# Optimization experiments

Measured on AMD Instinct MI355X. Metric: run time of the kernel, lower is better.

The kernel has to match this reference:

```python
import jax, jax.numpy as jnp
import numpy as np

HIDDEN_DIM = 64
EIGS_DIM = 16
N_LAYERS = 2
NUM_USERS = 100000
NUM_ITEMS = 200000
N_NODES = NUM_USERS + NUM_ITEMS
N_EDGES = 1250000
N_PATHS = 14  # 2**(sample_hop+1) - 2 with sample_hop=3
LN_EPS = 1e-5


def setup_inputs() -> dict:
    key = jax.random.key(0)
    k1, k2, k3, k4, k5 = jax.random.split(key, 5)
    return {
        "user_emb": 0.1 * jax.random.normal(k1, (NUM_USERS, HIDDEN_DIM), dtype=jnp.float32),
        "item_emb": 0.1 * jax.random.normal(k2, (NUM_ITEMS, HIDDEN_DIM), dtype=jnp.float32),
        "eigs": jax.random.normal(k3, (N_NODES, EIGS_DIM), dtype=jnp.float32),
        "lambda0": jnp.zeros((N_LAYERS,), dtype=jnp.float32),
        "path_emb_w": jnp.zeros((N_LAYERS, N_PATHS, 1), dtype=jnp.float32),
        "indices": jax.random.randint(k4, (2, N_EDGES), 0, N_NODES, dtype=jnp.int64)
        if jax.config.jax_enable_x64
        else jax.random.randint(k4, (2, N_EDGES), 0, N_NODES, dtype=jnp.int32),
        "path_type": jax.random.randint(k5, (N_EDGES,), 0, N_PATHS, dtype=jnp.int32),
    }


def _layer_norm(x, eps=LN_EPS):
    mu = jnp.mean(x, axis=-1, keepdims=True)
    var = jnp.var(x, axis=-1, keepdims=True)
    return (x - mu) * jax.lax.rsqrt(var + eps)


def _sparse_softmax(row, s, num_nodes):
    # softmax over edges grouped by target-node row index
    m = jax.ops.segment_max(s, row, num_segments=num_nodes)
    e = jnp.exp(s - m[row])
    denom = jax.ops.segment_sum(e, row, num_segments=num_nodes)
    return e / denom[row]


def _attention(y, eigs, row, col, path_type, lam0, pemb):
    sqrt_dim = 1.0 / jnp.sqrt(jnp.float32(HIDDEN_DIM))
    # per-edge q.k score  [E]
    x = jnp.sum(y[row] * y[col], axis=-1) * sqrt_dim
    yeig = jnp.sum(eigs[row] * eigs[col], axis=-1)
    s0 = x + jnp.exp(lam0) * yeig
    s1 = pemb[path_type, 0]
    a0 = _sparse_softmax(row, s0, N_NODES)
    a1 = _sparse_softmax(row, s1, N_NODES)
    a = 0.5 * (a0 + a1)
    # sparse-dense matmul: out[r] = sum_e a_e * v[col_e]
    return jax.ops.segment_sum(a[:, None] * y[col], row, num_segments=N_NODES)


def reference(user_emb, item_emb, eigs, lambda0, path_emb_w, indices, path_type):
    row, col = indices[0], indices[1]
    all_emb = jnp.concatenate([user_emb, item_emb], axis=0)  # [N, d]
    embs = [all_emb]
    for l in range(N_LAYERS):
        y = _layer_norm(all_emb)
        all_emb = _attention(y, eigs, row, col, path_type, lambda0[l], path_emb_w[l])
        embs.append(all_emb)
    light_out = jnp.mean(jnp.stack(embs, axis=1), axis=1)  # [N, d]
    return light_out
```

## Files before the change

### kernel.cpp

```cpp
#include <hip/hip_runtime.h>
#include <hip/hip_bf16.h>

#define HD 64
#define ED 16
#define NU 100000
#define NI 200000
#define NN 300000
#define NE 1250000
#define NP 14

#define RB 512
#define NBKT ((NN + RB - 1) / RB)
#define NR8 (NBKT * RB)
#define BCAP 2432
#define A_ITEMS 8
#define A_CHUNK (256 * A_ITEMS)
#define A_BLOCKS ((NE + A_CHUNK - 1) / A_CHUNK)
#define DBINS 64
#define IT 4

typedef __hip_bfloat16 bf16;
typedef unsigned short ushort8v __attribute__((ext_vector_type(8)));
typedef float  float4v __attribute__((ext_vector_type(4)));
typedef float  float2v __attribute__((ext_vector_type(2)));
typedef int    int2v   __attribute__((ext_vector_type(2)));

__device__ __forceinline__ float bf2f(unsigned short u) {
    union { unsigned int i; float f; } c; c.i = ((unsigned int)u) << 16; return c.f;
}
__device__ __forceinline__ unsigned short f2b(float x) {
    bf16 h = __float2bfloat16(x);
    unsigned short u; __builtin_memcpy(&u, &h, 2); return u;
}

__global__ void ln_kernel(const float* __restrict__ user_emb,
                          const float* __restrict__ item_emb,
                          bf16* __restrict__ yb)
{
    const int tid = blockIdx.x * blockDim.x + threadIdx.x;
    const int r   = tid >> 3;
    const int sub = tid & 7;
    if (r >= NN) return;
    const float* src = (r < NU) ? user_emb + (size_t)r * HD
                                : item_emb + (size_t)(r - NU) * HD;
    const float4 lo = *reinterpret_cast<const float4*>(src + sub * 8);
    const float4 hi = *reinterpret_cast<const float4*>(src + sub * 8 + 4);
    float x[8] = {lo.x, lo.y, lo.z, lo.w, hi.x, hi.y, hi.z, hi.w};

    float sm = 0.0f, sq = 0.0f;
#pragma unroll
    for (int j = 0; j < 8; ++j) { sm += x[j]; sq += x[j] * x[j]; }
    sm += __shfl_xor(sm, 1, 64); sq += __shfl_xor(sq, 1, 64);
    sm += __shfl_xor(sm, 2, 64); sq += __shfl_xor(sq, 2, 64);
    sm += __shfl_xor(sm, 4, 64); sq += __shfl_xor(sq, 4, 64);
    const float mu  = sm * (1.0f / 64.0f);
    const float var = sq * (1.0f / 64.0f) - mu * mu;
    const float inv = rsqrtf(var + 1e-5f);

    ushort8v w;
#pragma unroll
    for (int j = 0; j < 8; ++j) w[j] = f2b((x[j] - mu) * inv);
    *reinterpret_cast<ushort8v*>(yb + (size_t)r * HD + sub * 8) = w;
}

__global__ void bkt_scatter_kernel(const int* __restrict__ row,
                                   const int* __restrict__ col,
                                   const int* __restrict__ pt,
                                   int* __restrict__ wq_bkt,
                                   int* __restrict__ pairs)
{
    __shared__ int hist[NBKT];
    __shared__ int rbase[NBKT];
    __shared__ int roff[NBKT];
    const int tid = threadIdx.x;
    for (int j = tid; j < NBKT; j += 256) { hist[j] = 0; roff[j] = 0; }
    __syncthreads();

    const int base = blockIdx.x * A_CHUNK;
#pragma unroll
    for (int i = 0; i < A_ITEMS; ++i) {
        const int idx = base + i * 256 + tid;
        if (idx < NE) atomicAdd(&hist[row[idx] >> 9], 1);
    }
    __syncthreads();
    for (int j = tid; j < NBKT; j += 256) {
        const int h = hist[j];
        if (h) rbase[j] = atomicAdd(&wq_bkt[j], h);
    }
    __syncthreads();
#pragma unroll
    for (int i = 0; i < A_ITEMS; ++i) {
        const int idx = base + i * 256 + tid;
        if (idx < NE) {
            const int r = row[idx];
            const int b = r >> 9;
            const int v = col[idx] | (pt[idx] << 19) | ((r & (RB - 1)) << 23);
            const int o   = atomicAdd(&roff[b], 1);
            const int rel = rbase[b] + o;
            if (rel < BCAP) pairs[(size_t)b * BCAP + rel] = v;
        }
    }
}

__global__ __launch_bounds__(512)
void bkt_sort_kernel(const int* __restrict__ wq_bkt,
                     const int* __restrict__ pairs,
                     const float* __restrict__ eigs,
                     int2* __restrict__ rinfo,
                     int2* __restrict__ epacked)
{
    __shared__ int rcnt[RB], lrp[RB], wq2[RB], ssum[RB];
    __shared__ int dhist[DBINS], dbase[DBINS];
    __shared__ int perml[RB];
    __shared__ float estage[RB * ED];
    const int tid  = threadIdx.x;
    const int b    = blockIdx.x;
    const int r0   = b * RB;
    const int sbase = b * BCAP;
    int cntb = wq_bkt[b]; if (cntb > BCAP) cntb = BCAP;

    rcnt[tid] = 0; wq2[tid] = 0; perml[tid] = -1;
    if (tid < DBINS) dhist[tid] = 0;
    for (int k = tid; k < RB * ED; k += 512) {
        const int g = r0 * ED + k;
        estage[k] = (g < NN * ED) ? eigs[g] : 0.0f;
    }
    __syncthreads();

    for (int i = tid; i < cntb; i += 512)
        atomicAdd(&rcnt[(pairs[sbase + i] >> 23) & (RB - 1)], 1);
    __syncthreads();

    const int myc = rcnt[tid];
    ssum[tid] = myc;
    __syncthreads();
    for (int off = 1; off < RB; off <<= 1) {
        int x = (tid >= off) ? ssum[tid - off] : 0;
        __syncthreads();
        ssum[tid] += x;
        __syncthreads();
    }
    lrp[tid] = ssum[tid] - myc;
    __syncthreads();

    const int ra  = r0 + tid;
    const int bin = (DBINS - 1) - ((myc < DBINS - 1) ? myc : (DBINS - 1));
    if (ra < NN) atomicAdd(&dhist[bin], 1);
    __syncthreads();
    if (tid < DBINS) ssum[tid] = dhist[tid];
    __syncthreads();
    for (int off = 1; off < DBINS; off <<= 1) {
        int x = (tid < DBINS && tid >= off) ? ssum[tid - off] : 0;
        __syncthreads();
        if (tid < DBINS) ssum[tid] += x;
        __syncthreads();
    }
    if (tid < DBINS) { dbase[tid] = ssum[tid] - dhist[tid]; dhist[tid] = 0; }
    __syncthreads();
    if (ra < NN) perml[dbase[bin] + atomicAdd(&dhist[bin], 1)] = tid;
    __syncthreads();

    {
        const int j  = tid;
        const int R  = j >> 3, o = j & 7;
        const int N  = ((R & 3) << 4) | (R >> 2);
        const int pos = (N << 3) | o;
        const int rl = perml[j];
        int2 out;
        if (rl >= 0) {
            int dg = rcnt[rl]; if (dg > 0xFFF) dg = 0xFFF;
            out = make_int2(sbase + lrp[rl], (r0 + rl) | (dg << 19));
        } else {
            out = make_int2(0, -1);
        }
        rinfo[r0 + pos] = out;
    }

    for (int i = tid; i < cntb; i += 512) {
        const int v  = pairs[sbase + i];
        const int rl = (v >> 23) & (RB - 1);
        const int c  = v & 0x7FFFF;
        const float4* ep = reinterpret_cast<const float4*>(eigs + (size_t)c * ED);
        const float4 q0 = ep[0], q1 = ep[1], q2 = ep[2], q3 = ep[3];
        const float* er = estage + rl * ED;
        float d = q0.x * er[0]  + q0.y * er[1]  + q0.z * er[2]  + q0.w * er[3]
                + q1.x * er[4]  + q1.y * er[5]  + q1.z * er[6]  + q1.w * er[7]
                + q2.x * er[8]  + q2.y * er[9]  + q2.z * er[10] + q2.w * er[11]
                + q3.x * er[12] + q3.y * er[13] + q3.z * er[14] + q3.w * er[15];
        const int o   = atomicAdd(&wq2[rl], 1);
        const int pos = sbase + lrp[rl] + o;
        epacked[pos] = make_int2(v & 0x7FFFFF, __float_as_int(d));
    }
}

template <int LAYER>
__global__ __launch_bounds__(256, 4)
void attn_row_kernel(const bf16* __restrict__ yb,
                     const int2* __restrict__ rinfo,
                     const int2* __restrict__ epacked,
                     const float* __restrict__ lambda0,
                     const float* __restrict__ pemb,
                     const float* __restrict__ user_emb,
                     const float* __restrict__ item_emb,
                     bf16* __restrict__ yb_next,
                     float* __restrict__ lntab,
                     float* __restrict__ io)
{
    __shared__ float e1tab[NP];
    if (threadIdx.x < NP)
        e1tab[threadIdx.x] = __expf(pemb[LAYER * NP + threadIdx.x]);
    __syncthreads();

    const int tid  = (int)threadIdx.x;
    const int gl   = tid >> 3;
    const int sub  = tid & 7;
    const int lane = tid & 63;
    const int base = (int)blockIdx.x * (32 * IT);

    const float lam = __expf(lambda0[LAYER]);
    const bf16*  ybs = yb + (size_t)sub * 8;
    const int2v* ep2 = reinterpret_cast<const int2v*>(epacked);

    int2 ri[IT];
#pragma unroll
    for (int it = 0; it < IT; ++it) ri[it] = rinfo[base + it * 32 + gl];

    int2v myv_n;
    {
        const int2v* mp = ep2 + ri[0].x + sub;
        asm volatile("global_load_dwordx2 %0, %1, off" : "=v"(myv_n) : "v"(mp));
        asm volatile("s_waitcnt vmcnt(0)" : "+v"(myv_n));
    }

#pragma unroll
    for (int it = 0; it < IT; ++it) {
        const int2 ric   = ri[it];
        const bool valid = (ric.y >= 0);
        const int r      = valid ? (ric.y & 0x7FFFF) : 0;
        const int deg    = valid ? ((ric.y >> 19) & 0xFFF) : 0;
        const int start  = ric.x;

        int2v myv = myv_n;
        if (sub >= deg) { myv[0] = 0; myv[1] = 0; }

        int   vv[8];
        float ee[8];
#pragma unroll
        for (int kk = 0; kk < 8; ++kk) {
            const int src = (lane & ~7) + kk;
            vv[kk] = __shfl(myv[0], src, 64);
            ee[kk] = __int_as_float(__shfl(myv[1], src, 64));
        }
        const int nb = (deg < 8) ? deg : 8;

        ushort8v yru;
        float4v em_lo = {0,0,0,0}, em_hi = {0,0,0,0};
        float2v ms = {0,0};
        {
            const bf16* yp = ybs + (size_t)r * HD;
            asm volatile("global_load_dwordx4 %0, %1, off" : "=v"(yru) : "v"(yp));
            if (LAYER == 1) {
                const float* ep = ((r < NU) ? user_emb + (size_t)r * HD
                                            : item_emb + (size_t)(r - NU) * HD) + sub * 8;
                asm volatile("global_load_dwordx4 %0, %1, off" : "=v"(em_lo) : "v"(ep));
                asm volatile("global_load_dwordx4 %0, %1, off" : "=v"(em_hi) : "v"(ep + 4));
                const float* tp = lntab + 2 * (size_t)r;
                asm volatile("global_load_dwordx2 %0, %1, off" : "=v"(ms) : "v"(tp));
            }
        }

        const bf16* p0 = ybs + (size_t)(vv[0] & 0x7FFFF) * HD;
        const bf16* p1 = ybs + (size_t)(vv[1] & 0x7FFFF) * HD;
        const bf16* p2 = ybs + (size_t)(vv[2] & 0x7FFFF) * HD;
        const bf16* p3 = ybs + (size_t)(vv[3] & 0x7FFFF) * HD;
        const bf16* p4 = ybs + (size_t)(vv[4] & 0x7FFFF) * HD;
        const bf16* p5 = ybs + (size_t)(vv[5] & 0x7FFFF) * HD;
        const bf16* p6 = ybs + (size_t)(vv[6] & 0x7FFFF) * HD;
        const bf16* p7 = ybs + (size_t)(vv[7] & 0x7FFFF) * HD;
        ushort8v u0, u1, u2, u3, u4, u5, u6, u7;
        asm volatile("global_load_dwordx4 %0, %1, off" : "=v"(u0) : "v"(p0));
        asm volatile("global_load_dwordx4 %0, %1, off" : "=v"(u1) : "v"(p1));
        asm volatile("global_load_dwordx4 %0, %1, off" : "=v"(u2) : "v"(p2));
        asm volatile("global_load_dwordx4 %0, %1, off" : "=v"(u3) : "v"(p3));
        asm volatile("global_load_dwordx4 %0, %1, off" : "=v"(u4) : "v"(p4));
        asm volatile("global_load_dwordx4 %0, %1, off" : "=v"(u5) : "v"(p5));
        asm volatile("global_load_dwordx4 %0, %1, off" : "=v"(u6) : "v"(p6));
        asm volatile("global_load_dwordx4 %0, %1, off" : "=v"(u7) : "v"(p7));

        if (it + 1 < IT) {
            const int2v* mp = ep2 + ri[it + 1].x + sub;
            asm volatile("global_load_dwordx2 %0, %1, off" : "=v"(myv_n) : "v"(mp));
        }

        asm volatile("s_waitcnt vmcnt(0)"
                     : "+v"(u0), "+v"(u1), "+v"(u2), "+v"(u3),
                       "+v"(u4), "+v"(u5), "+v"(u6), "+v"(u7),
                       "+v"(yru), "+v"(em_lo), "+v"(em_hi), "+v"(ms), "+v"(myv_n));

        float yrf[8];
#pragma unroll
        for (int j = 0; j < 8; ++j) yrf[j] = bf2f(yru[j]);

        float U0[8], U1[8];
#pragma unroll
        for (int j = 0; j < 8; ++j) { U0[j] = 0.0f; U1[j] = 0.0f; }
        float d0 = 0.0f, d1 = 0.0f;

        auto consume = [&](const ushort8v& uc, int vk, float ek) {
            float yc[8];
            float sdot = 0.0f;
#pragma unroll
            for (int j = 0; j < 8; ++j) { yc[j] = bf2f(uc[j]); sdot += yrf[j] * yc[j]; }
            sdot += __shfl_xor(sdot, 1, 64);
            sdot += __shfl_xor(sdot, 2, 64);
            sdot += __shfl_xor(sdot, 4, 64);
            const float e0 = __expf(sdot * 0.125f + lam * ek);
            const float e1 = e1tab[(vk >> 19) & 15];
            d0 += e0; d1 += e1;
#pragma unroll
            for (int j = 0; j < 8; ++j) {
                U0[j] += e0 * yc[j];
                U1[j] += e1 * yc[j];
            }
        };
        if (nb > 0) consume(u0, vv[0], ee[0]);
        if (nb > 1) consume(u1, vv[1], ee[1]);
        if (nb > 2) consume(u2, vv[2], ee[2]);
        if (nb > 3) consume(u3, vv[3], ee[3]);
        if (nb > 4) consume(u4, vv[4], ee[4]);
        if (nb > 5) consume(u5, vv[5], ee[5]);
        if (nb > 6) consume(u6, vv[6], ee[6]);
        if (nb > 7) consume(u7, vv[7], ee[7]);

        for (int k0 = 8; k0 < deg; k0 += 8) {
            int2 mv = ((k0 + sub) < deg) ? epacked[start + k0 + sub]
                                         : make_int2(0, 0);
            int   vv2[8];
            float ee2[8];
#pragma unroll
            for (int kk = 0; kk < 8; ++kk) {
                const int src = (lane & ~7) + kk;
                vv2[kk] = __shfl(mv.x, src, 64);
                ee2[kk] = __int_as_float(__shfl(mv.y, src, 64));
            }
            const int nb2 = ((deg - k0) < 8) ? (deg - k0) : 8;
#pragma unroll
            for (int kk = 0; kk < 8; ++kk) {
                if (kk < nb2) {
                    ushort8v uc = *reinterpret_cast<const ushort8v*>(
                        ybs + (size_t)(vv2[kk] & 0x7FFFF) * HD);
                    consume(uc, vv2[kk], ee2[kk]);
                }
            }
        }

        const float i0 = deg ? 0.5f / d0 : 0.0f;
        const float i1 = deg ? 0.5f / d1 : 0.0f;
        float acc[8];
#pragma unroll
        for (int j = 0; j < 8; ++j) acc[j] = i0 * U0[j] + i1 * U1[j];

        if (LAYER == 0) {
            if (valid) {
                float sm = 0.0f, sq = 0.0f;
#pragma unroll
                for (int j = 0; j < 8; ++j) { sm += acc[j]; sq += acc[j] * acc[j]; }
                sm += __shfl_xor(sm, 1, 64); sq += __shfl_xor(sq, 1, 64);
                sm += __shfl_xor(sm, 2, 64); sq += __shfl_xor(sq, 2, 64);
                sm += __shfl_xor(sm, 4, 64); sq += __shfl_xor(sq, 4, 64);
                const float mu  = sm * (1.0f / 64.0f);
                const float var = sq * (1.0f / 64.0f) - mu * mu;
                const float inv = rsqrtf(var + 1e-5f);
                ushort8v w;
#pragma unroll
                for (int j = 0; j < 8; ++j) w[j] = f2b((acc[j] - mu) * inv);
                *reinterpret_cast<ushort8v*>(yb_next + (size_t)r * HD + sub * 8) = w;
                if (sub == 0) {
                    float2v t; t[0] = mu; t[1] = sqrtf(var + 1e-5f);
                    *reinterpret_cast<float2v*>(lntab + 2 * (size_t)r) = t;
                }
            }
        } else {
            if (valid) {
                float* iorow = io + (size_t)r * HD + sub * 8;
                const float third = 1.0f / 3.0f;
                float4v o0, o1;
#pragma unroll
                for (int j = 0; j < 4; ++j) {
                    const float out1 = yrf[j] * ms[1] + ms[0];
                    o0[j] = (em_lo[j] + out1 + acc[j]) * third;
                }
#pragma unroll
                for (int j = 0; j < 4; ++j) {
                    const float out1 = yrf[j + 4] * ms[1] + ms[0];
                    o1[j] = (em_hi[j] + out1 + acc[j + 4]) * third;
                }
                *reinterpret_cast<float4v*>(iorow)     = o0;
                *reinterpret_cast<float4v*>(iorow + 4) = o1;
            }
        }
    }
}

extern "C" void kernel_launch(void* const* d_in, const int* in_sizes, int n_in,
                              void* d_out, int out_size, void* d_ws, size_t ws_size,
                              hipStream_t stream)
{
    const float* user_emb = (const float*)d_in[0];
    const float* item_emb = (const float*)d_in[1];
    const float* eigs     = (const float*)d_in[2];
    const float* lambda0  = (const float*)d_in[3];
    const float* pemb     = (const float*)d_in[4];
    const int*   indices  = (const int*)d_in[5];
    const int*   ptype    = (const int*)d_in[6];
    const int*   row = indices;
    const int*   col = indices + NE;

    float* io = (float*)d_out;
    char*  ws = (char*)d_ws;
    bf16*  yb      = (bf16*)ws;
    bf16*  yb2     = yb + (size_t)NN * HD;
    int*   pairs   = (int*)(yb2 + (size_t)NN * HD);
    int2*  epacked = (int2*)(pairs + (size_t)NBKT * BCAP);
    int2*  rinfo   = epacked + (size_t)NBKT * BCAP;
    float* lntab   = (float*)(rinfo + NR8);
    int*   wq_bkt  = (int*)(lntab + 2 * (size_t)NN);

    const dim3 blk(256);
    const int gridAttn = NR8 / (32 * IT);

    ln_kernel<<<(NN * 8 + 255) / 256, blk, 0, stream>>>(user_emb, item_emb, yb);

    hipMemsetAsync(wq_bkt, 0, NBKT * sizeof(int), stream);
    bkt_scatter_kernel<<<A_BLOCKS, blk, 0, stream>>>(row, col, ptype, wq_bkt, pairs);
    bkt_sort_kernel<<<NBKT, dim3(512), 0, stream>>>(wq_bkt, pairs, eigs, rinfo, epacked);

    attn_row_kernel<0><<<gridAttn, blk, 0, stream>>>(yb, rinfo, epacked,
                                                     lambda0, pemb, user_emb,
                                                     item_emb, yb2, lntab, io);
    attn_row_kernel<1><<<gridAttn, blk, 0, stream>>>(yb2, rinfo, epacked,
                                                     lambda0, pemb, user_emb,
                                                     item_emb, nullptr, lntab, io);
}
```

Before: 355.3 us.

## Fuse layernorm, bucket scatter and bucket sort into one cooperative kernel

Merges the layernorm, memset, edge bucket scatter and per-bucket sort/eig-dot stages into a single cooperative kernel that separates phases with grid-wide syncs, replacing four launches. The aim is to cut launch overhead and the gaps between dependent kernels in the preprocessing stage. The scatter phase now has one block per bucket (586 blocks of 512 threads) working on contiguous edge chunks, in place of the earlier A_BLOCKS grid. The design needs all blocks to be co-resident, with a fallback to the old multi-kernel path if the cooperative launch fails. Grid syncs and the changed scatter parallelism could offset the gains.

```diff
diff --git a/kernel.cpp b/kernel.cpp
--- a/kernel.cpp
+++ b/kernel.cpp
@@ -1,5 +1,8 @@
 #include <hip/hip_runtime.h>
 #include <hip/hip_bf16.h>
+#include <hip/hip_cooperative_groups.h>
+
+namespace cg = cooperative_groups;
 
 #define HD 64
 #define ED 16
@@ -16,6 +19,7 @@
 #define A_ITEMS 8
 #define A_CHUNK (256 * A_ITEMS)
 #define A_BLOCKS ((NE + A_CHUNK - 1) / A_CHUNK)
+#define ECH ((NE + NBKT - 1) / NBKT)
 #define DBINS 64
 #define IT 4
 
@@ -33,14 +37,10 @@
     unsigned short u; __builtin_memcpy(&u, &h, 2); return u;
 }
 
-__global__ void ln_kernel(const float* __restrict__ user_emb,
-                          const float* __restrict__ item_emb,
-                          bf16* __restrict__ yb)
+__device__ __forceinline__ void ln_row(const float* __restrict__ user_emb,
+                                       const float* __restrict__ item_emb,
+                                       bf16* __restrict__ yb, int r, int sub)
 {
-    const int tid = blockIdx.x * blockDim.x + threadIdx.x;
-    const int r   = tid >> 3;
-    const int sub = tid & 7;
-    if (r >= NN) return;
     const float* src = (r < NU) ? user_emb + (size_t)r * HD
                                 : item_emb + (size_t)(r - NU) * HD;
     const float4 lo = *reinterpret_cast<const float4*>(src + sub * 8);
@@ -61,6 +61,153 @@
 #pragma unroll
     for (int j = 0; j < 8; ++j) w[j] = f2b((x[j] - mu) * inv);
     *reinterpret_cast<ushort8v*>(yb + (size_t)r * HD + sub * 8) = w;
+}
+
+__global__ __launch_bounds__(512, 8)
+void build_kernel(const float* __restrict__ user_emb,
+                  const float* __restrict__ item_emb,
+                  const float* __restrict__ eigs,
+                  const int* __restrict__ row,
+                  const int* __restrict__ col,
+                  const int* __restrict__ pt,
+                  bf16* __restrict__ yb,
+                  int* __restrict__ wq_bkt,
+                  int* __restrict__ pairs,
+                  int2* __restrict__ rinfo,
+                  int2* __restrict__ epacked)
+{
+    __shared__ int rcnt[RB], lrp[RB], wq2[RB], ssum[RB];
+    __shared__ int dhist[DBINS], dbase[DBINS];
+    __shared__ int perml[RB];
+    __shared__ float estage[RB * ED];
+    int* hist  = (int*)estage;
+    int* rbase = hist + NBKT;
+    int* roff  = rbase + NBKT;
+
+    const int tid = (int)threadIdx.x;
+    const int b   = (int)blockIdx.x;
+    cg::grid_group grid = cg::this_grid();
+
+    for (int j = b * 512 + tid; j < NBKT; j += NBKT * 512) wq_bkt[j] = 0;
+    {
+        const int sub = tid & 7;
+        const int rg  = tid >> 3;
+#pragma unroll
+        for (int p = 0; p < 8; ++p) {
+            const int r = b * RB + p * 64 + rg;
+            if (r < NN) ln_row(user_emb, item_emb, yb, r, sub);
+        }
+    }
+    grid.sync();
+
+    for (int j = tid; j < NBKT; j += 512) { hist[j] = 0; roff[j] = 0; }
+    __syncthreads();
+    const int e0 = b * ECH;
+    const int e1 = (e0 + ECH < NE) ? e0 + ECH : NE;
+    for (int i = e0 + tid; i < e1; i += 512)
+        atomicAdd(&hist[row[i] >> 9], 1);
+    __syncthreads();
+    for (int j = tid; j < NBKT; j += 512) {
+        const int h = hist[j];
+        if (h) rbase[j] = atomicAdd(&wq_bkt[j], h);
+    }
+    __syncthreads();
+    for (int i = e0 + tid; i < e1; i += 512) {
+        const int r  = row[i];
+        const int bb = r >> 9;
+        const int v  = col[i] | (pt[i] << 19) | ((r & (RB - 1)) << 23);
+        const int o   = atomicAdd(&roff[bb], 1);
+        const int rel = rbase[bb] + o;
+        if (rel < BCAP) pairs[(size_t)bb * BCAP + rel] = v;
+    }
+    grid.sync();
+
+    const int r0    = b * RB;
+    const int sbase = b * BCAP;
+    int cntb = wq_bkt[b]; if (cntb > BCAP) cntb = BCAP;
+
+    rcnt[tid] = 0; wq2[tid] = 0; perml[tid] = -1;
+    if (tid < DBINS) dhist[tid] = 0;
+    for (int k = tid; k < RB * ED; k += 512) {
+        const int g = r0 * ED + k;
+        estage[k] = (g < NN * ED) ? eigs[g] : 0.0f;
+    }
+    __syncthreads();
+
+    for (int i = tid; i < cntb; i += 512)
+        atomicAdd(&rcnt[(pairs[sbase + i] >> 23) & (RB - 1)], 1);
+    __syncthreads();
+
+    const int myc = rcnt[tid];
+    ssum[tid] = myc;
+    __syncthreads();
+    for (int off = 1; off < RB; off <<= 1) {
+        int x = (tid >= off) ? ssum[tid - off] : 0;
+        __syncthreads();
+        ssum[tid] += x;
+        __syncthreads();
+    }
+    lrp[tid] = ssum[tid] - myc;
+    __syncthreads();
+
+    const int ra  = r0 + tid;
+    const int bin = (DBINS - 1) - ((myc < DBINS - 1) ? myc : (DBINS - 1));
+    if (ra < NN) atomicAdd(&dhist[bin], 1);
+    __syncthreads();
+    if (tid < DBINS) ssum[tid] = dhist[tid];
+    __syncthreads();
+    for (int off = 1; off < DBINS; off <<= 1) {
+        int x = (tid < DBINS && tid >= off) ? ssum[tid - off] : 0;
+        __syncthreads();
+        if (tid < DBINS) ssum[tid] += x;
+        __syncthreads();
+    }
+    if (tid < DBINS) { dbase[tid] = ssum[tid] - dhist[tid]; dhist[tid] = 0; }
+    __syncthreads();
+    if (ra < NN) perml[dbase[bin] + atomicAdd(&dhist[bin], 1)] = tid;
+    __syncthreads();
+
+    {
+        const int j  = tid;
+        const int R  = j >> 3, o = j & 7;
+        const int N  = ((R & 3) << 4) | (R >> 2);
+        const int pos = (N << 3) | o;
+        const int rl = perml[j];
+        int2 out;
+        if (rl >= 0) {
+            int dg = rcnt[rl]; if (dg > 0xFFF) dg = 0xFFF;
+            out = make_int2(sbase + lrp[rl], (r0 + rl) | (dg << 19));
+        } else {
+            out = make_int2(0, -1);
+        }
+        rinfo[r0 + pos] = out;
+    }
+
+    for (int i = tid; i < cntb; i += 512) {
+        const int v  = pairs[sbase + i];
+        const int rl = (v >> 23) & (RB - 1);
+        const int c  = v & 0x7FFFF;
+        const float4* ep = reinterpret_cast<const float4*>(eigs + (size_t)c * ED);
+        const float4 q0 = ep[0], q1 = ep[1], q2 = ep[2], q3 = ep[3];
+        const float* er = estage + rl * ED;
+        float d = q0.x * er[0]  + q0.y * er[1]  + q0.z * er[2]  + q0.w * er[3]
+                + q1.x * er[4]  + q1.y * er[5]  + q1.z * er[6]  + q1.w * er[7]
+                + q2.x * er[8]  + q2.y * er[9]  + q2.z * er[10] + q2.w * er[11]
+                + q3.x * er[12] + q3.y * er[13] + q3.z * er[14] + q3.w * er[15];
+        const int o   = atomicAdd(&wq2[rl], 1);
+        const int pos = sbase + lrp[rl] + o;
+        epacked[pos] = make_int2(v & 0x7FFFFF, __float_as_int(d));
+    }
+}
+
+__global__ void ln_kernel(const float* __restrict__ user_emb,
+                          const float* __restrict__ item_emb,
+                          bf16* __restrict__ yb)
+{
+    const int tid = blockIdx.x * blockDim.x + threadIdx.x;
+    const int r   = tid >> 3;
+    if (r >= NN) return;
+    ln_row(user_emb, item_emb, yb, r, tid & 7);
 }
 
 __global__ void bkt_scatter_kernel(const int* __restrict__ row,
@@ -429,11 +576,23 @@
     const dim3 blk(256);
     const int gridAttn = NR8 / (32 * IT);
 
-    ln_kernel<<<(NN * 8 + 255) / 256, blk, 0, stream>>>(user_emb, item_emb, yb);
-
-    hipMemsetAsync(wq_bkt, 0, NBKT * sizeof(int), stream);
-    bkt_scatter_kernel<<<A_BLOCKS, blk, 0, stream>>>(row, col, ptype, wq_bkt, pairs);
-    bkt_sort_kernel<<<NBKT, dim3(512), 0, stream>>>(wq_bkt, pairs, eigs, rinfo, epacked);
+    bool coop_ok;
+    {
+        void* args[] = {(void*)&user_emb, (void*)&item_emb, (void*)&eigs,
+                        (void*)&row, (void*)&col, (void*)&ptype,
+                        (void*)&yb, (void*)&wq_bkt, (void*)&pairs,
+                        (void*)&rinfo, (void*)&epacked};
+        hipError_t e = hipLaunchCooperativeKernel((const void*)build_kernel,
+                                                  dim3(NBKT), dim3(512),
+                                                  args, 0, stream);
+        coop_ok = (e == hipSuccess);
+    }
+    if (!coop_ok) {
+        hipMemsetAsync(wq_bkt, 0, NBKT * sizeof(int), stream);
+        ln_kernel<<<(NN * 8 + 255) / 256, blk, 0, stream>>>(user_emb, item_emb, yb);
+        bkt_scatter_kernel<<<A_BLOCKS, blk, 0, stream>>>(row, col, ptype, wq_bkt, pairs);
+        bkt_sort_kernel<<<NBKT, dim3(512), 0, stream>>>(wq_bkt, pairs, eigs, rinfo, epacked);
+    }
 
     attn_row_kernel<0><<<gridAttn, blk, 0, stream>>>(yb, rinfo, epacked,
                                                      lambda0, pemb, user_emb,
```

Measured after the change: 520.0 us. 46.3% more time.
